# Optimization experiments

Measured on AMD Instinct MI355X. Metric: run time of the kernel, lower is better.

The kernel has to match this reference:

```python
import jax, jax.numpy as jnp
import numpy as np

VIEW_NUM = 360
CHAN_NUM = 512
BATCH = 2
IMG = 512


def setup_inputs() -> dict:
    key = jax.random.key(0)
    x = jax.random.normal(key, (BATCH, 1, IMG, IMG), dtype=jnp.float32)
    return {"x": x}


def _bilinear_sample_zeros(img, ix, iy):
    """Bilinear sample img (B,1,H,W) at pixel coords ix, iy (H,W), zeros padding.
    Matches F.grid_sample(mode='bilinear', padding_mode='zeros', align_corners=False)."""
    H, W = img.shape[-2], img.shape[-1]
    x0 = jnp.floor(ix)
    y0 = jnp.floor(iy)
    x1 = x0 + 1.0
    y1 = y0 + 1.0
    wx1 = ix - x0
    wx0 = 1.0 - wx1
    wy1 = iy - y0
    wy0 = 1.0 - wy1

    def gather(yy, xx):
        valid = (xx >= 0) & (xx <= W - 1) & (yy >= 0) & (yy <= H - 1)
        xi = jnp.clip(xx, 0, W - 1).astype(jnp.int32)
        yi = jnp.clip(yy, 0, H - 1).astype(jnp.int32)
        # fancy-index over spatial dims -> (B,1,H,W)
        return img[:, :, yi, xi] * valid.astype(img.dtype)

    return (gather(y0, x0) * (wy0 * wx0)
            + gather(y0, x1) * (wy0 * wx1)
            + gather(y1, x0) * (wy1 * wx0)
            + gather(y1, x1) * (wy1 * wx1))


def _fp(x):
    B, C, H, W = x.shape
    # affine_grid base coords, align_corners=False: (2i+1)/N - 1
    bx = (2.0 * jnp.arange(W, dtype=x.dtype) + 1.0) / W - 1.0
    by = (2.0 * jnp.arange(H, dtype=x.dtype) + 1.0) / H - 1.0
    X = bx[None, :]  # (1,W)
    Y = by[:, None]  # (H,1)
    i = jnp.arange(VIEW_NUM, dtype=x.dtype)
    angles = -jnp.pi * (i + 1.0) / VIEW_NUM - jnp.pi
    cosv = jnp.cos(angles)
    sinv = jnp.sin(angles)

    def per_view(carry, cs):
        c, s = cs
        # theta = [[c,-s,0],[s,c,0]]; grid = base @ theta^T
        gx = c * X - s * Y  # (H,W) normalized sample x
        gy = s * X + c * Y  # (H,W) normalized sample y
        # unnormalize (align_corners=False)
        ix = ((gx + 1.0) * W - 1.0) * 0.5
        iy = ((gy + 1.0) * H - 1.0) * 0.5
        samp = _bilinear_sample_zeros(x, ix, iy)  # (B,1,H,W)
        return carry, jnp.sum(samp, axis=2)  # sum over height -> (B,1,W)

    _, cols = jax.lax.scan(per_view, 0, (cosv, sinv))  # (V,B,1,W)
    sino = jnp.transpose(cols, (1, 2, 3, 0)) * 0.5  # (B,1,chanNum,viewNum)
    return sino


def reference(x):
    return _fp(x)
```

## Files before the change

kernel.cpp:

```cpp
#include <hip/hip_runtime.h>

typedef __fp16 h2 __attribute__((ext_vector_type(2)));

constexpr int VIEWS = 360;
constexpr int IMGSZ = 512;
constexpr int WCHUNK = 64;
constexpr int KH = 64;
constexpr int NXF4 = 25;
constexpr int PITCH = 100;
constexpr int MAXNY = 94;
constexpr int PW = 712;
constexpr int PH = 704;
constexpr int PAD = 96;

__global__ __launch_bounds__(256) void pad_kernel(const float* __restrict__ x,
                                                  unsigned* __restrict__ padq) {
    constexpr int PW4 = PW / 4;
    constexpr int total = PH * PW4;
    int idx = blockIdx.x * 256 + threadIdx.x;
    if (idx >= total) return;
    int py = idx / PW4;
    int px4 = idx - py * PW4;
    int gx = px4 * 4 - PAD;
    int gy = py - PAD;
    const float* img0 = x;
    const float* img1 = x + (size_t)IMGSZ * IMGSZ;
    float4 a = make_float4(0.f, 0.f, 0.f, 0.f);
    float4 bq = a;
    if ((unsigned)gy < (unsigned)IMGSZ && (unsigned)gx < (unsigned)IMGSZ) {
        size_t off = (size_t)gy * IMGSZ + gx;
        a  = *(const float4*)(img0 + off);
        bq = *(const float4*)(img1 + off);
    }
    uint4 d;
    d.x = __builtin_bit_cast(unsigned, __builtin_amdgcn_cvt_pkrtz(a.x, bq.x));
    d.y = __builtin_bit_cast(unsigned, __builtin_amdgcn_cvt_pkrtz(a.y, bq.y));
    d.z = __builtin_bit_cast(unsigned, __builtin_amdgcn_cvt_pkrtz(a.z, bq.z));
    d.w = __builtin_bit_cast(unsigned, __builtin_amdgcn_cvt_pkrtz(a.w, bq.w));
    *(uint4*)&padq[(size_t)idx * 4] = d;
}

__global__ __launch_bounds__(256) void fp_kernel(const unsigned* __restrict__ padq,
                                                 float* __restrict__ out) {
    __shared__ __align__(16) unsigned tileU[PITCH * MAXNY];

    int blk = blockIdx.x;
    int wc = blk & 7;
    int v = blk >> 3;

    int tid = threadIdx.x;
    int lane = tid & 63;
    int g = tid >> 6;
    int w = wc * WCHUNK + lane;

    double ang = -3.14159265358979323846 * (double)(v + 1) / (double)VIEWS
                 - 3.14159265358979323846;
    float c = (float)cos(ang);
    float s = (float)sin(ang);

    float xw = (float)w + 0.5f - 256.0f;
    float cxw = fmaf(c, xw, 255.5f);
    float sxw = fmaf(s, xw, 255.5f);

    float lo = -1e30f, hi = 1e30f;
    {
        float coef = -s, base = cxw;
        if (fabsf(coef) > 1e-6f) {
            float a = (-1.0f - base) / coef;
            float bq = (512.0f - base) / coef;
            lo = fmaxf(lo, fminf(a, bq));
            hi = fminf(hi, fmaxf(a, bq));
        } else if (!(base > -1.0f && base < 512.0f)) {
            lo = 1e30f; hi = -1e30f;
        }
    }
    {
        float coef = c, base = sxw;
        if (fabsf(coef) > 1e-6f) {
            float a = (-1.0f - base) / coef;
            float bq = (512.0f - base) / coef;
            lo = fmaxf(lo, fminf(a, bq));
            hi = fminf(hi, fmaxf(a, bq));
        } else if (!(base > -1.0f && base < 512.0f)) {
            lo = 1e30f; hi = -1e30f;
        }
    }
    float h0f = fminf(fmaxf(floorf(lo + 255.5f) - 1.0f, 0.0f), 512.0f);
    float h1f = fminf(fmaxf(ceilf(hi + 255.5f) + 1.0f, -1.0f), 511.0f);
    int h0 = (int)h0f;
    int h1 = (int)h1f;

    int bh0 = h0, bh1 = h1;
    #pragma unroll
    for (int m = 1; m < 64; m <<= 1) {
        bh0 = min(bh0, __shfl_xor(bh0, m, 64));
        bh1 = max(bh1, __shfl_xor(bh1, m, 64));
    }

    float xa = (float)(wc * WCHUNK) + 0.5f - 256.0f;
    float xb = xa + 63.0f;

    float acc0 = 0.0f, acc1 = 0.0f;
    float step4x = -4.0f * s;
    float step4y = 4.0f * c;

    for (int hc = bh0; hc <= bh1; hc += KH) {
        int hend = min(hc + KH - 1, bh1);

        float ha = (float)hc - 255.5f;
        float hb = (float)hend - 255.5f;
        float ix00 = c * xa - s * ha, ix01 = c * xa - s * hb;
        float ix10 = c * xb - s * ha, ix11 = c * xb - s * hb;
        float iy00 = s * xa + c * ha, iy01 = s * xa + c * hb;
        float iy10 = s * xb + c * ha, iy11 = s * xb + c * hb;
        float ixmn = fminf(fminf(ix00, ix01), fminf(ix10, ix11)) + 255.5f;
        float iymn = fminf(fminf(iy00, iy01), fminf(iy10, iy11)) + 255.5f;
        float iymx = fmaxf(fmaxf(iy00, iy01), fmaxf(iy10, iy11)) + 255.5f;
        int x_lo = (int)floorf(ixmn) - 1;
        int x_lo4 = x_lo & ~3;
        int y_lo = (int)floorf(iymn) - 1;
        int NY = min((int)floorf(iymx) + 3 - y_lo, MAXNY);
        int total4 = NY * NXF4;
        int nit = (total4 + 255) >> 8;

        __syncthreads();

        {
            const unsigned* pb = padq + (y_lo + PAD) * PW + (x_lo4 + PAD);
            for (int k = 0; k < nit; ++k) {
                int i = (k << 8) + tid;
                int ic = min(i, total4 - 1);
                int ry = ic / NXF4;
                uint4 val = *(const uint4*)(pb + 4 * ic + (PW - 4 * NXF4) * ry);
                *(uint4*)&tileU[ic << 2] = val;
            }
        }
        __syncthreads();

        float hh0 = (float)(hc + g) - 255.5f;
        float ixr = fmaf(-s, hh0, cxw) - (float)x_lo4;
        float iyr = fmaf(c, hh0, sxw) - (float)y_lo;
        h2 accp0 = (h2)0.0f;
        h2 accp1 = (h2)0.0f;
        int parity = 0;
        #pragma unroll 4
        for (int h = hc + g; h <= hend; h += 4) {
            float fx = floorf(ixr);
            float fy = floorf(iyr);
            int lx = (int)fx;
            int ly = (int)fy;
            float wx1 = ixr - fx;
            float wy1 = iyr - fy;
            h2 wxs = __builtin_amdgcn_cvt_pkrtz(wx1, wx1);
            h2 wys = __builtin_amdgcn_cvt_pkrtz(wy1, wy1);
            const unsigned* p = tileU + (ly * PITCH + lx);
            h2 t00 = __builtin_bit_cast(h2, p[0]);
            h2 t01 = __builtin_bit_cast(h2, p[1]);
            h2 t10 = __builtin_bit_cast(h2, p[PITCH]);
            h2 t11 = __builtin_bit_cast(h2, p[PITCH + 1]);
            h2 r0 = t00 + (t01 - t00) * wxs;
            h2 r1 = t10 + (t11 - t10) * wxs;
            h2 contrib = r0 + (r1 - r0) * wys;
            if (parity) accp1 += contrib; else accp0 += contrib;
            parity ^= 1;
            ixr += step4x;
            iyr += step4y;
        }
        acc0 += (float)accp0.x + (float)accp1.x;
        acc1 += (float)accp0.y + (float)accp1.y;
    }

    __syncthreads();
    tileU[(g << 6) + lane] = __float_as_uint(acc0);
    tileU[256 + (g << 6) + lane] = __float_as_uint(acc1);
    __syncthreads();
    if (g == 0) {
        float r0 = __uint_as_float(tileU[lane]) + __uint_as_float(tileU[64 + lane]) +
                   __uint_as_float(tileU[128 + lane]) + __uint_as_float(tileU[192 + lane]);
        float r1 = __uint_as_float(tileU[256 + lane]) + __uint_as_float(tileU[320 + lane]) +
                   __uint_as_float(tileU[384 + lane]) + __uint_as_float(tileU[448 + lane]);
        size_t o = (size_t)w * VIEWS + v;
        out[o] = r0 * 0.5f;
        out[(size_t)IMGSZ * VIEWS + o] = r1 * 0.5f;
    }
}

extern "C" void kernel_launch(void* const* d_in, const int* in_sizes, int n_in,
                              void* d_out, int out_size, void* d_ws, size_t ws_size,
                              hipStream_t stream) {
    const float* x = (const float*)d_in[0];
    float* out = (float*)d_out;
    unsigned* padq = (unsigned*)d_ws;

    constexpr int padTotal = PH * (PW / 4);
    pad_kernel<<<(padTotal + 255) / 256, 256, 0, stream>>>(x, padq);

    int nblocks = VIEWS * (IMGSZ / WCHUNK);
    fp_kernel<<<nblocks, 256, 0, stream>>>(padq, out);
}
```

Before: 154.4 us.

## Pick per-view LDS tile pitch to avoid bank conflicts and use async global-to-LDS copies

For each view, the kernel now tries several LDS row pitches (100 to 112 floats) and scores how rows separated by the sample step map onto LDS banks. It keeps the pitch with the lowest score and computes the row index with a magic-number multiply in place of an integer divide. Full wavefronts stage the tile with global_load_lds async copies, while partial wavefronts fall back to ordinary loads and stores. The inner sampling loop is unrolled 8 instead of 4. The aim is to cut LDS bank conflicts in the gather and the cost of staging, at the price of a runtime-variable pitch and an extra vmcnt wait.

```diff
diff --git a/kernel.cpp b/kernel.cpp
--- a/kernel.cpp
+++ b/kernel.cpp
@@ -6,12 +6,16 @@
 constexpr int IMGSZ = 512;
 constexpr int WCHUNK = 64;
 constexpr int KH = 64;
-constexpr int NXF4 = 25;
-constexpr int PITCH = 100;
 constexpr int MAXNY = 94;
+constexpr int LDSDW = 9800;
 constexpr int PW = 712;
 constexpr int PH = 704;
 constexpr int PAD = 96;
+
+#define ASYNC_CP16(SRC, DST)                                              \
+    __builtin_amdgcn_global_load_lds(                                     \
+        (const __attribute__((address_space(1))) unsigned*)(SRC),         \
+        (__attribute__((address_space(3))) unsigned*)(DST), 16, 0, 0)
 
 __global__ __launch_bounds__(256) void pad_kernel(const float* __restrict__ x,
                                                   unsigned* __restrict__ padq) {
@@ -42,7 +46,7 @@
 
 __global__ __launch_bounds__(256) void fp_kernel(const unsigned* __restrict__ padq,
                                                  float* __restrict__ out) {
-    __shared__ __align__(16) unsigned tileU[PITCH * MAXNY];
+    __shared__ __align__(16) unsigned tileU[LDSDW];
 
     int blk = blockIdx.x;
     int wc = blk & 7;
@@ -57,6 +61,34 @@
                  - 3.14159265358979323846;
     float c = (float)cos(ang);
     float s = (float)sin(ang);
+
+    int NYbb = min((int)(63.0f * (fabsf(s) + fabsf(c))) + 6, MAXNY);
+    int bestj = 0, bestsc = 1000;
+#pragma unroll
+    for (int j = 0; j < 4; ++j) {
+        int Pj = 100 + 4 * j;
+        if (Pj * NYbb > LDSDW) break;
+        float t = fmaf((float)Pj, s, c);
+        float rm = rintf(t);
+        float dl = fabsf(t - rm);
+        int m = (int)rm;
+        int am = m & 31;
+        int sc;
+        if (am & 1)              sc = 0;
+        else if (m == 0)         sc = 1;
+        else if (dl >= 0.22f)    sc = 2;
+        else if ((am & 3) == 2)  sc = 2;
+        else if ((am & 7) == 4)  sc = 4;
+        else if ((am & 15) == 8) sc = 6;
+        else if (am == 16)       sc = 8;
+        else                     sc = 10;
+        if (sc < bestsc) { bestsc = sc; bestj = j; }
+    }
+    int P = 100 + 4 * bestj;
+    int NXW = P >> 2;
+    unsigned mgc = (bestj == 0) ? 10486u : (bestj == 1) ? 10083u
+                 : (bestj == 2) ? 9710u : 9363u;
+    int stepRow = PW - P;
 
     float xw = (float)w + 0.5f - 256.0f;
     float cxw = fmaf(c, xw, 255.5f);
@@ -120,7 +152,7 @@
         int x_lo4 = x_lo & ~3;
         int y_lo = (int)floorf(iymn) - 1;
         int NY = min((int)floorf(iymx) + 3 - y_lo, MAXNY);
-        int total4 = NY * NXF4;
+        int total4 = NY * NXW;
         int nit = (total4 + 255) >> 8;
 
         __syncthreads();
@@ -129,12 +161,17 @@
             const unsigned* pb = padq + (y_lo + PAD) * PW + (x_lo4 + PAD);
             for (int k = 0; k < nit; ++k) {
                 int i = (k << 8) + tid;
-                int ic = min(i, total4 - 1);
-                int ry = ic / NXF4;
-                uint4 val = *(const uint4*)(pb + 4 * ic + (PW - 4 * NXF4) * ry);
-                *(uint4*)&tileU[ic << 2] = val;
+                if (((k << 8) + (g << 6) + 63) < total4) {
+                    unsigned ry = ((unsigned)i * mgc) >> 18;
+                    ASYNC_CP16(pb + 4 * i + stepRow * (int)ry, &tileU[i << 2]);
+                } else if (i < total4) {
+                    unsigned ry = ((unsigned)i * mgc) >> 18;
+                    uint4 val = *(const uint4*)(pb + 4 * i + stepRow * (int)ry);
+                    *(uint4*)&tileU[i << 2] = val;
+                }
             }
         }
+        asm volatile("s_waitcnt vmcnt(0)" ::: "memory");
         __syncthreads();
 
         float hh0 = (float)(hc + g) - 255.5f;
@@ -143,7 +180,7 @@
         h2 accp0 = (h2)0.0f;
         h2 accp1 = (h2)0.0f;
         int parity = 0;
-        #pragma unroll 4
+        #pragma unroll 8
         for (int h = hc + g; h <= hend; h += 4) {
             float fx = floorf(ixr);
             float fy = floorf(iyr);
@@ -153,11 +190,12 @@
             float wy1 = iyr - fy;
             h2 wxs = __builtin_amdgcn_cvt_pkrtz(wx1, wx1);
             h2 wys = __builtin_amdgcn_cvt_pkrtz(wy1, wy1);
-            const unsigned* p = tileU + (ly * PITCH + lx);
+            const unsigned* p = tileU + (ly * P + lx);
+            const unsigned* q = p + P;
             h2 t00 = __builtin_bit_cast(h2, p[0]);
             h2 t01 = __builtin_bit_cast(h2, p[1]);
-            h2 t10 = __builtin_bit_cast(h2, p[PITCH]);
-            h2 t11 = __builtin_bit_cast(h2, p[PITCH + 1]);
+            h2 t10 = __builtin_bit_cast(h2, q[0]);
+            h2 t11 = __builtin_bit_cast(h2, q[1]);
             h2 r0 = t00 + (t01 - t00) * wxs;
             h2 r1 = t10 + (t11 - t10) * wxs;
             h2 contrib = r0 + (r1 - r0) * wys;
```

New measurement: 153.6 us. No clear change (-0.5%).

## Pad LDS tile pitch to avoid bank conflicts and batch tile loads with fixed trip count

Applied to the files above, without the earlier changes.

Changes the LDS tile pitch from 100 to 101 dwords so the bilinear gathers spread across more banks. To fit the odd pitch, the tile fill becomes a fixed-count loop that issues all global loads first and then stores them as scalar dwords, ordered row-major within each column group. The inner sampling loop now uses a hardware fract and truncation instead of floor, unrolls 8 instead of 4, and launch bounds request 4 blocks per CU. Truncation matches floor only for non-negative coordinates, and each load pass now always covers 96 rows, clamping to the last row instead of stopping at NY.

```diff
diff --git a/kernel.cpp b/kernel.cpp
--- a/kernel.cpp
+++ b/kernel.cpp
@@ -6,12 +6,15 @@
 constexpr int IMGSZ = 512;
 constexpr int WCHUNK = 64;
 constexpr int KH = 64;
-constexpr int NXF4 = 25;
-constexpr int PITCH = 100;
+constexpr int PITCH = 101;
 constexpr int MAXNY = 94;
+constexpr int LDSDW = PITCH * MAXNY;
 constexpr int PW = 712;
 constexpr int PH = 704;
 constexpr int PAD = 96;
+constexpr int RJOBS = 96;
+constexpr int KJOBS = 25;
+constexpr int NIT = (RJOBS * KJOBS + 255) / 256;
 
 __global__ __launch_bounds__(256) void pad_kernel(const float* __restrict__ x,
                                                   unsigned* __restrict__ padq) {
@@ -40,9 +43,9 @@
     *(uint4*)&padq[(size_t)idx * 4] = d;
 }
 
-__global__ __launch_bounds__(256) void fp_kernel(const unsigned* __restrict__ padq,
-                                                 float* __restrict__ out) {
-    __shared__ __align__(16) unsigned tileU[PITCH * MAXNY];
+__global__ __launch_bounds__(256, 4) void fp_kernel(const unsigned* __restrict__ padq,
+                                                    float* __restrict__ out) {
+    __shared__ __align__(16) unsigned tileU[LDSDW];
 
     int blk = blockIdx.x;
     int wc = blk & 7;
@@ -120,19 +123,31 @@
         int x_lo4 = x_lo & ~3;
         int y_lo = (int)floorf(iymn) - 1;
         int NY = min((int)floorf(iymx) + 3 - y_lo, MAXNY);
-        int total4 = NY * NXF4;
-        int nit = (total4 + 255) >> 8;
 
         __syncthreads();
 
         {
             const unsigned* pb = padq + (y_lo + PAD) * PW + (x_lo4 + PAD);
-            for (int k = 0; k < nit; ++k) {
-                int i = (k << 8) + tid;
-                int ic = min(i, total4 - 1);
-                int ry = ic / NXF4;
-                uint4 val = *(const uint4*)(pb + 4 * ic + (PW - 4 * NXF4) * ry);
-                *(uint4*)&tileU[ic << 2] = val;
+            uint4 vals[NIT];
+            #pragma unroll
+            for (int it = 0; it < NIT; ++it) {
+                int j = min(it * 256 + tid, RJOBS * KJOBS - 1);
+                int k = j / RJOBS;
+                int r = j - k * RJOBS;
+                int rr = min(r, NY - 1);
+                vals[it] = *(const uint4*)(pb + rr * PW + (k << 2));
+            }
+            #pragma unroll
+            for (int it = 0; it < NIT; ++it) {
+                int j = min(it * 256 + tid, RJOBS * KJOBS - 1);
+                int k = j / RJOBS;
+                int r = j - k * RJOBS;
+                int rr = min(r, NY - 1);
+                int base = rr * PITCH + (k << 2);
+                tileU[base + 0] = vals[it].x;
+                tileU[base + 1] = vals[it].y;
+                tileU[base + 2] = vals[it].z;
+                tileU[base + 3] = vals[it].w;
             }
         }
         __syncthreads();
@@ -143,14 +158,12 @@
         h2 accp0 = (h2)0.0f;
         h2 accp1 = (h2)0.0f;
         int parity = 0;
-        #pragma unroll 4
+        #pragma unroll 8
         for (int h = hc + g; h <= hend; h += 4) {
-            float fx = floorf(ixr);
-            float fy = floorf(iyr);
-            int lx = (int)fx;
-            int ly = (int)fy;
-            float wx1 = ixr - fx;
-            float wy1 = iyr - fy;
+            int lx = (int)ixr;
+            int ly = (int)iyr;
+            float wx1 = __builtin_amdgcn_fractf(ixr);
+            float wy1 = __builtin_amdgcn_fractf(iyr);
             h2 wxs = __builtin_amdgcn_cvt_pkrtz(wx1, wx1);
             h2 wys = __builtin_amdgcn_cvt_pkrtz(wy1, wy1);
             const unsigned* p = tileU + (ly * PITCH + lx);
```

Result: no change. 152.6 us (-1.1%).

## Exploit view symmetry to compute two views per sample pass via DPP row sums

Applied to the files above, without the earlier changes.

Launches only half the views and derives each mirrored view (v+180) from the same bilinear samples. Each sample's contribution is summed across the wavefront with DPP row reductions and atomically added into the output column of the paired view. Also replaces floor with trunc and folds the tile address into one fma, and raises the inner-loop unroll to 8. This trades half the sampling work for a DPP reduction plus global atomics on every row step. It relies on the output being zero-initialised before the atomics, which this code does not do, and trunc only matches floor for non-negative coordinates.

```diff
diff --git a/kernel.cpp b/kernel.cpp
--- a/kernel.cpp
+++ b/kernel.cpp
@@ -40,13 +40,38 @@
     *(uint4*)&padq[(size_t)idx * 4] = d;
 }
 
-__global__ __launch_bounds__(256) void fp_kernel(const unsigned* __restrict__ padq,
-                                                 float* __restrict__ out) {
+__device__ __forceinline__ h2 dpp_reduce_add_h2(h2 x) {
+    h2 acc = x;
+#define DPP_STEP(ctrl)                                                      \
+    {                                                                       \
+        int t = __builtin_amdgcn_update_dpp(                                \
+            0, (int)__builtin_bit_cast(unsigned, acc), (ctrl), 0xf, 0xf,    \
+            true);                                                          \
+        acc = acc + __builtin_bit_cast(h2, (unsigned)t);                    \
+    }
+    DPP_STEP(0x111)
+    DPP_STEP(0x112)
+    DPP_STEP(0x114)
+    DPP_STEP(0x118)
+    DPP_STEP(0x142)
+    DPP_STEP(0x143)
+#undef DPP_STEP
+    return acc;
+}
+
+__device__ __forceinline__ void gatomic_fadd(float* p, float v) {
+    asm volatile("global_atomic_add_f32 %0, %1, off" : : "v"(p), "v"(v)
+                 : "memory");
+}
+
+__global__ __launch_bounds__(256, 4) void fp_kernel(const unsigned* __restrict__ padq,
+                                                    float* __restrict__ out) {
     __shared__ __align__(16) unsigned tileU[PITCH * MAXNY];
 
     int blk = blockIdx.x;
     int wc = blk & 7;
     int v = blk >> 3;
+    int vj = v + 180;
 
     int tid = threadIdx.x;
     int lane = tid & 63;
@@ -128,8 +153,7 @@
         {
             const unsigned* pb = padq + (y_lo + PAD) * PW + (x_lo4 + PAD);
             for (int k = 0; k < nit; ++k) {
-                int i = (k << 8) + tid;
-                int ic = min(i, total4 - 1);
+                int ic = min((k << 8) + tid, total4 - 1);
                 int ry = ic / NXF4;
                 uint4 val = *(const uint4*)(pb + 4 * ic + (PW - 4 * NXF4) * ry);
                 *(uint4*)&tileU[ic << 2] = val;
@@ -143,17 +167,16 @@
         h2 accp0 = (h2)0.0f;
         h2 accp1 = (h2)0.0f;
         int parity = 0;
-        #pragma unroll 4
+        #pragma unroll 8
         for (int h = hc + g; h <= hend; h += 4) {
-            float fx = floorf(ixr);
-            float fy = floorf(iyr);
-            int lx = (int)fx;
-            int ly = (int)fy;
-            float wx1 = ixr - fx;
-            float wy1 = iyr - fy;
+            float tx = truncf(ixr);
+            float ty = truncf(iyr);
+            float wx1 = ixr - tx;
+            float wy1 = iyr - ty;
             h2 wxs = __builtin_amdgcn_cvt_pkrtz(wx1, wx1);
             h2 wys = __builtin_amdgcn_cvt_pkrtz(wy1, wy1);
-            const unsigned* p = tileU + (ly * PITCH + lx);
+            unsigned a = (unsigned)fmaf(ty, 400.0f, tx * 4.0f);
+            const unsigned* p = (const unsigned*)((const char*)tileU + a);
             h2 t00 = __builtin_bit_cast(h2, p[0]);
             h2 t01 = __builtin_bit_cast(h2, p[1]);
             h2 t10 = __builtin_bit_cast(h2, p[PITCH]);
@@ -163,6 +186,12 @@
             h2 contrib = r0 + (r1 - r0) * wys;
             if (parity) accp1 += contrib; else accp0 += contrib;
             parity ^= 1;
+            h2 red = dpp_reduce_add_h2(contrib);
+            if (lane == 63 && __builtin_bit_cast(unsigned, red) != 0u) {
+                float* p0 = out + ((size_t)(511 - h) * VIEWS + vj);
+                gatomic_fadd(p0, (float)red.x * 0.5f);
+                gatomic_fadd(p0 + (size_t)IMGSZ * VIEWS, (float)red.y * 0.5f);
+            }
             ixr += step4x;
             iyr += step4y;
         }
@@ -195,6 +224,6 @@
     constexpr int padTotal = PH * (PW / 4);
     pad_kernel<<<(padTotal + 255) / 256, 256, 0, stream>>>(x, padq);
 
-    int nblocks = VIEWS * (IMGSZ / WCHUNK);
+    int nblocks = (VIEWS / 2) * (IMGSZ / WCHUNK);
     fp_kernel<<<nblocks, 256, 0, stream>>>(padq, out);
 }
```

Measured after the change: 180.9 us. 17.2% more time.
